# Kernel optimization log

Hardware: AMD Instinct MI355X
Metric: run time of the kernel (lower is better)

## Reference

```python
import jax, jax.numpy as jnp
import numpy as np

N_NODES = 50000
N_EDGES = 800000
N_FEAT = 128
DIM = 64
N_GRAPHS = 512


def setup_inputs() -> dict:
    key = jax.random.key(0)
    k1, k2, k3, k4, k5, k6 = jax.random.split(key, 6)
    x = jax.random.normal(k1, (N_NODES, N_FEAT), dtype=jnp.float32)
    edge_index = jax.random.randint(k2, (2, N_EDGES), 0, N_NODES, dtype=jnp.int64)
    batch = jnp.sort(jax.random.randint(k3, (N_NODES,), 0, N_GRAPHS, dtype=jnp.int64))
    W1 = jax.random.normal(k4, (N_FEAT, DIM), dtype=jnp.float32) * 0.05
    W2 = jax.random.normal(k5, (DIM, DIM), dtype=jnp.float32) * 0.05
    Wfc = jax.random.normal(k6, (DIM, 1), dtype=jnp.float32) * 0.05
    return {"x": x, "edge_index": edge_index, "batch": batch,
            "W1": W1, "W2": W2, "Wfc": Wfc}


def _gcn_conv(h, src, dst, W):
    # GCNConv(normalize=False, bias=False): linear transform then scatter-add
    # over edges: out[dst] += (h @ W)[src]
    h = jnp.einsum('nf,fd->nd', h, W)
    return jax.ops.segment_sum(h[src], dst, num_segments=N_NODES)


def reference(x, edge_index, batch, W1, W2, Wfc):
    src, dst = edge_index[0], edge_index[1]
    h = jax.nn.relu(_gcn_conv(x, src, dst, W1))          # [N, DIM]
    h = _gcn_conv(h, src, dst, W2)                        # [N, DIM]
    # global_mean_pool over graph ids
    counts = jax.ops.segment_sum(jnp.ones((N_NODES,), h.dtype), batch,
                                 num_segments=N_GRAPHS)   # [G]
    pooled = jax.ops.segment_sum(h, batch, num_segments=N_GRAPHS)
    pooled = pooled / jnp.maximum(counts, 1.0)[:, None]   # [G, DIM]
    return jax.nn.sigmoid(pooled @ Wfc)                   # [G, 1]
```

## Files before the change

### kernel.cpp

```cpp
#include <hip/hip_runtime.h>
#include <cmath>

#define N_NODES 50000
#define N_EDGES 800000
#define N_FEAT 128
#define DIM 64
#define N_GRAPHS 512
#define GGRID ((N_NODES + 63) / 64)
#define NBKT GGRID
#define BH_BLK 128
#define EPB (N_EDGES / BH_BLK)
#define NCNT (NBKT * BH_BLK)
#define P2_NBLK ((NCNT + 511) / 512)
#define BKT_CAP 2048

__device__ __forceinline__ unsigned short f2bf(float f) {
  union { float f; unsigned int u; } v; v.f = f;
  return (unsigned short)((v.u + 0x7FFFu + ((v.u >> 16) & 1u)) >> 16);
}
__device__ __forceinline__ float bf2f(unsigned short u) {
  union { unsigned int u; float f; } v; v.u = (unsigned int)u << 16;
  return v.f;
}

__global__ __launch_bounds__(256) void bhist_w2fc(const int* __restrict__ dst,
                                                  int* __restrict__ cnt,
                                                  const float* __restrict__ W2,
                                                  const float* __restrict__ Wfc,
                                                  float* __restrict__ w2fc) {
  if (blockIdx.x == BH_BLK) {
    int k = threadIdx.x;
    if (k < 64) {
      float s = 0.f;
#pragma unroll 8
      for (int j = 0; j < 64; j++) s += W2[k * 64 + j] * Wfc[j];
      w2fc[k] = s;
    }
    return;
  }
  __shared__ int lh[NBKT];
  const int tid = threadIdx.x, k = blockIdx.x;
  for (int i = tid; i < NBKT; i += 256) lh[i] = 0;
  __syncthreads();
  const int base = k * EPB;
  for (int j = tid; j < EPB; j += 256)
    atomicAdd(&lh[dst[base + j] >> 6], 1);
  __syncthreads();
  for (int i = tid; i < NBKT; i += 256) cnt[i * BH_BLK + k] = lh[i];
}

__global__ __launch_bounds__(512) void psum512(const int* __restrict__ cnt,
                                               int* __restrict__ partials) {
  __shared__ int ws[8];
  int gid = blockIdx.x * 512 + threadIdx.x;
  int v = (gid < NCNT) ? cnt[gid] : 0;
#pragma unroll
  for (int off = 32; off; off >>= 1) v += __shfl_down(v, off, 64);
  int lane = threadIdx.x & 63, w = threadIdx.x >> 6;
  if (lane == 0) ws[w] = v;
  __syncthreads();
  if (threadIdx.x == 0) {
    int s = 0;
#pragma unroll
    for (int i = 0; i < 8; i++) s += ws[i];
    partials[blockIdx.x] = s;
  }
}

__global__ __launch_bounds__(256) void scan_partials(int* __restrict__ partials) {
  __shared__ int buf[256];
  int tid = threadIdx.x;
  int v = (tid < P2_NBLK) ? partials[tid] : 0;
  buf[tid] = v;
  __syncthreads();
  for (int off = 1; off < 256; off <<= 1) {
    int t = (tid >= off) ? buf[tid - off] : 0;
    __syncthreads();
    buf[tid] += t;
    __syncthreads();
  }
  if (tid < P2_NBLK) partials[tid] = buf[tid] - v;
}

__global__ __launch_bounds__(512) void sblocks512(int* __restrict__ cnt,
                                                  const int* __restrict__ partials,
                                                  int* __restrict__ bucket_ptr) {
  __shared__ int buf[512];
  int tid = threadIdx.x;
  int gid = blockIdx.x * 512 + tid;
  int v = (gid < NCNT) ? cnt[gid] : 0;
  buf[tid] = v;
  __syncthreads();
  for (int off = 1; off < 512; off <<= 1) {
    int t = (tid >= off) ? buf[tid - off] : 0;
    __syncthreads();
    buf[tid] += t;
    __syncthreads();
  }
  int excl = buf[tid] - v + partials[blockIdx.x];
  if (gid < NCNT) {
    cnt[gid] = excl;
    if ((gid & (BH_BLK - 1)) == 0) bucket_ptr[gid / BH_BLK] = excl;
    if (gid == NCNT - 1) bucket_ptr[NBKT] = excl + v;
  }
}

template<int K>
__device__ __forceinline__ void gemm_body_bf(const float* __restrict__ A,
                                             const float* __restrict__ W,
                                             unsigned short* __restrict__ out,
                                             int M, int row0, int tid,
                                             float* sX, float* sW) {
  const int tx = tid & 15, ty = tid >> 4;
  const int q = tid & 7, r0 = tid >> 3;
  float acc[4][4] = {};

  for (int kb = 0; kb < K; kb += 32) {
    __syncthreads();
    if ((kb & 63) == 0) {
#pragma unroll
      for (int i = 0; i < 16; i++)
        sW[i * 256 + tid] = W[kb * 64 + i * 256 + tid];
    }
#pragma unroll
    for (int rr = 0; rr < 64; rr += 32) {
      int r = r0 + rr;
      int gr = row0 + r;
      float4 v = make_float4(0.f, 0.f, 0.f, 0.f);
      if (gr < M) v = *(const float4*)&A[(size_t)gr * K + kb + q * 4];
      *(float4*)&sX[r * 36 + q * 4] = v;
    }
    __syncthreads();

    const int kw = kb & 63;
#pragma unroll 4
    for (int k = 0; k < 32; k += 4) {
      float4 wv[4];
#pragma unroll
      for (int kk = 0; kk < 4; kk++)
        wv[kk] = *(const float4*)&sW[(kw + k + kk) * 64 + tx * 4];
#pragma unroll
      for (int r = 0; r < 4; r++) {
        float4 xv = *(const float4*)&sX[(ty * 4 + r) * 36 + k];
        const float xs[4] = {xv.x, xv.y, xv.z, xv.w};
#pragma unroll
        for (int kk = 0; kk < 4; kk++) {
          acc[r][0] += xs[kk] * wv[kk].x;
          acc[r][1] += xs[kk] * wv[kk].y;
          acc[r][2] += xs[kk] * wv[kk].z;
          acc[r][3] += xs[kk] * wv[kk].w;
        }
      }
    }
  }

#pragma unroll
  for (int r = 0; r < 4; r++) {
    int gr = row0 + ty * 4 + r;
    if (gr < M) {
      ushort4 u;
      u.x = f2bf(acc[r][0]); u.y = f2bf(acc[r][1]);
      u.z = f2bf(acc[r][2]); u.w = f2bf(acc[r][3]);
      *(ushort4*)&out[(size_t)gr * 64 + tx * 4] = u;
    }
  }
}

__global__ __launch_bounds__(256) void gemm1_bscatter(
    const float* __restrict__ x, const float* __restrict__ W1,
    unsigned short* __restrict__ h1, const int* __restrict__ src,
    const int* __restrict__ dst, const int* __restrict__ cnt,
    unsigned int* __restrict__ ebuf) {
  __shared__ float sX[64 * 36];
  __shared__ float sW[64 * 64];
  const int tid = threadIdx.x;
  if (blockIdx.x < GGRID) {
    gemm_body_bf<N_FEAT>(x, W1, h1, N_NODES, blockIdx.x * 64, tid, sX, sW);
  } else {
    int* loff = (int*)sX;
    const int k = blockIdx.x - GGRID;
    for (int i = tid; i < NBKT; i += 256) loff[i] = cnt[i * BH_BLK + k];
    __syncthreads();
    const int base = k * EPB;
    for (int j = tid; j < EPB; j += 256) {
      int e = base + j;
      int d = dst[e];
      int pos = atomicAdd(&loff[d >> 6], 1);
      ebuf[pos] = ((unsigned int)src[e] << 6) | (unsigned int)(d & 63);
    }
  }
}

__global__ __launch_bounds__(1024, 8) void gather_z_fused(
    const unsigned short* __restrict__ h1,
    const unsigned int* __restrict__ ebuf,
    const int* __restrict__ bucket_ptr,
    const float* __restrict__ w2fc,
    float* __restrict__ z) {
  __shared__ int colL[BKT_CAP];
  __shared__ int lstart[64];
  __shared__ int lcur[64];
  __shared__ float sw[64];
  const int tid = threadIdx.x;
  const int b = blockIdx.x;
  const int p0 = bucket_ptr[b];
  int cnt = bucket_ptr[b + 1] - p0;
  if (cnt > BKT_CAP) cnt = BKT_CAP;

  if (tid < 64) { lstart[tid] = 0; sw[tid] = w2fc[tid]; }
  __syncthreads();
  for (int i = tid; i < cnt; i += 1024)
    atomicAdd(&lstart[ebuf[p0 + i] & 63], 1);
  __syncthreads();
  if (tid < 64) {
    int v = lstart[tid], s = v;
#pragma unroll
    for (int off = 1; off < 64; off <<= 1) {
      int t = __shfl_up(s, off, 64);
      if (tid >= off) s += t;
    }
    lstart[tid] = s - v;
    lcur[tid] = s - v;
  }
  __syncthreads();
  for (int i = tid; i < cnt; i += 1024) {
    unsigned int u = ebuf[p0 + i];
    int pos = atomicAdd(&lcur[u & 63], 1);
    colL[pos] = (int)(u >> 6);
  }
  __syncthreads();

  const int lane = tid & 63, w = tid >> 6;
  const int eo = lane >> 4, qfo = (lane & 15) << 2;
#pragma unroll
  for (int ni = 0; ni < 4; ni++) {
    const int r = ni * 16 + w;
    const int i1 = lcur[r];
    int i = lstart[r];
    float4 acc = make_float4(0.f, 0.f, 0.f, 0.f);
    for (; i + 16 <= i1; i += 16) {
      int s0 = colL[i + eo];
      int s1 = colL[i + 4 + eo];
      int s2 = colL[i + 8 + eo];
      int s3 = colL[i + 12 + eo];
      ushort4 u0 = *(const ushort4*)&h1[(size_t)s0 * 64 + qfo];
      ushort4 u1 = *(const ushort4*)&h1[(size_t)s1 * 64 + qfo];
      ushort4 u2 = *(const ushort4*)&h1[(size_t)s2 * 64 + qfo];
      ushort4 u3 = *(const ushort4*)&h1[(size_t)s3 * 64 + qfo];
      acc.x += (bf2f(u0.x) + bf2f(u1.x)) + (bf2f(u2.x) + bf2f(u3.x));
      acc.y += (bf2f(u0.y) + bf2f(u1.y)) + (bf2f(u2.y) + bf2f(u3.y));
      acc.z += (bf2f(u0.z) + bf2f(u1.z)) + (bf2f(u2.z) + bf2f(u3.z));
      acc.w += (bf2f(u0.w) + bf2f(u1.w)) + (bf2f(u2.w) + bf2f(u3.w));
    }
    for (; i + 4 <= i1; i += 4) {
      int s = colL[i + eo];
      ushort4 u = *(const ushort4*)&h1[(size_t)s * 64 + qfo];
      acc.x += bf2f(u.x); acc.y += bf2f(u.y);
      acc.z += bf2f(u.z); acc.w += bf2f(u.w);
    }
    if (eo < i1 - i) {
      int s = colL[i + eo];
      ushort4 u = *(const ushort4*)&h1[(size_t)s * 64 + qfo];
      acc.x += bf2f(u.x); acc.y += bf2f(u.y);
      acc.z += bf2f(u.z); acc.w += bf2f(u.w);
    }
#pragma unroll
    for (int m = 16; m <= 32; m <<= 1) {
      acc.x += __shfl_xor(acc.x, m, 64);
      acc.y += __shfl_xor(acc.y, m, 64);
      acc.z += __shfl_xor(acc.z, m, 64);
      acc.w += __shfl_xor(acc.w, m, 64);
    }
    float p = fmaxf(acc.x, 0.f) * sw[qfo] + fmaxf(acc.y, 0.f) * sw[qfo + 1] +
              fmaxf(acc.z, 0.f) * sw[qfo + 2] + fmaxf(acc.w, 0.f) * sw[qfo + 3];
#pragma unroll
    for (int m = 1; m <= 8; m <<= 1) p += __shfl_xor(p, m, 64);
    int node = b * 64 + r;
    if (lane == 0 && node < N_NODES) z[node] = p;
  }
}

__global__ __launch_bounds__(256) void graph_pool(const float* __restrict__ z,
                                                  const unsigned int* __restrict__ ebuf,
                                                  const int* __restrict__ bucket_ptr,
                                                  const int* __restrict__ batch,
                                                  float* __restrict__ out) {
  __shared__ float sacc[4];
  int g = blockIdx.x;
  int tid = threadIdx.x, lane = tid & 63, w = tid >> 6;

  int lo = 0, hi = N_NODES;
  while (lo < hi) { int mid = (lo + hi) >> 1; if (batch[mid] < g) lo = mid + 1; else hi = mid; }
  const int start = lo;
  hi = N_NODES;
  while (lo < hi) { int mid = (lo + hi) >> 1; if (batch[mid] < g + 1) lo = mid + 1; else hi = mid; }
  const int end = lo;

  float s = 0.f;
  if (end > start) {
    const int b0 = start >> 6, b1 = ((end - 1) >> 6) + 1;
    for (int b = b0; b < b1; b++) {
      const int q0 = bucket_ptr[b], q1 = bucket_ptr[b + 1];
      const int base = b << 6;
      for (int i = q0 + tid; i < q1; i += 256) {
        unsigned int u = ebuf[i];
        int d = base + (int)(u & 63);
        if (d >= start && d < end) s += z[u >> 6];
      }
    }
  }
#pragma unroll
  for (int off = 32; off; off >>= 1) s += __shfl_down(s, off, 64);
  if (lane == 0) sacc[w] = s;
  __syncthreads();
  if (tid == 0) {
    float v = sacc[0] + sacc[1] + sacc[2] + sacc[3];
    v /= fmaxf((float)(end - start), 1.f);
    out[g] = 1.f / (1.f + expf(-v));
  }
}

extern "C" void kernel_launch(void* const* d_in, const int* in_sizes, int n_in,
                              void* d_out, int out_size, void* d_ws, size_t ws_size,
                              hipStream_t stream) {
  const float* x     = (const float*)d_in[0];
  const int*   ei    = (const int*)d_in[1];
  const int*   batch = (const int*)d_in[2];
  const float* W1    = (const float*)d_in[3];
  const float* W2    = (const float*)d_in[4];
  const float* Wfc   = (const float*)d_in[5];
  float*       out   = (float*)d_out;

  const int* src = ei;
  const int* dst = ei + N_EDGES;

  char* ws = (char*)d_ws;
  unsigned short* h1 = (unsigned short*)(ws);
  float* z    = (float*)(ws + (size_t)N_NODES * DIM * 2);
  float* w2fc = z + N_NODES;
  int*   cnt  = (int*)(w2fc + 64);
  int*   partials = cnt + NCNT;
  unsigned int* ebuf = (unsigned int*)(partials + P2_NBLK);
  int*   bucket_ptr  = (int*)(ebuf + N_EDGES);

  bhist_w2fc<<<BH_BLK + 1, 256, 0, stream>>>(dst, cnt, W2, Wfc, w2fc);
  psum512<<<P2_NBLK, 512, 0, stream>>>(cnt, partials);
  scan_partials<<<1, 256, 0, stream>>>(partials);
  sblocks512<<<P2_NBLK, 512, 0, stream>>>(cnt, partials, bucket_ptr);

  gemm1_bscatter<<<GGRID + BH_BLK, 256, 0, stream>>>(x, W1, h1, src, dst, cnt, ebuf);

  gather_z_fused<<<NBKT, 1024, 0, stream>>>(h1, ebuf, bucket_ptr, w2fc, z);

  graph_pool<<<N_GRAPHS, 256, 0, stream>>>(z, ebuf, bucket_ptr, batch, out);
}
```

Measured before the change: 151.4 us.

## Spread GEMM1 tiles across the sort-preparation kernels and merge the partial scan

Splits the 782 GEMM1 row tiles across the histogram, partial-sum, block-scan and scatter launches, so the otherwise underfilled small kernels also do matrix work alongside their main job. The separate single-block partials scan is removed; each scan block now recomputes the prefix over the partials itself. The count reduction and scan switch to 256-thread blocks that each handle two counters via int2 loads. The tile split is hardcoded (262+160+160+200 = 782) and must match GGRID exactly, and the scan blocks repeat work on the partials.

New measurement: 159.6 us. 1.05x slower.

```diff
diff --git a/kernel.cpp b/kernel.cpp
--- a/kernel.cpp
+++ b/kernel.cpp
@@ -14,6 +14,11 @@
 #define P2_NBLK ((NCNT + 511) / 512)
 #define BKT_CAP 2048
 
+#define T_BHIST 262
+#define T_PSUM  160
+#define T_SBLK  160
+#define T_BSCAT 200
+
 __device__ __forceinline__ unsigned short f2bf(float f) {
   union { float f; unsigned int u; } v; v.f = f;
   return (unsigned short)((v.u + 0x7FFFu + ((v.u >> 16) & 1u)) >> 16);
@@ -21,88 +26,6 @@
 __device__ __forceinline__ float bf2f(unsigned short u) {
   union { unsigned int u; float f; } v; v.u = (unsigned int)u << 16;
   return v.f;
-}
-
-__global__ __launch_bounds__(256) void bhist_w2fc(const int* __restrict__ dst,
-                                                  int* __restrict__ cnt,
-                                                  const float* __restrict__ W2,
-                                                  const float* __restrict__ Wfc,
-                                                  float* __restrict__ w2fc) {
-  if (blockIdx.x == BH_BLK) {
-    int k = threadIdx.x;
-    if (k < 64) {
-      float s = 0.f;
-#pragma unroll 8
-      for (int j = 0; j < 64; j++) s += W2[k * 64 + j] * Wfc[j];
-      w2fc[k] = s;
-    }
-    return;
-  }
-  __shared__ int lh[NBKT];
-  const int tid = threadIdx.x, k = blockIdx.x;
-  for (int i = tid; i < NBKT; i += 256) lh[i] = 0;
-  __syncthreads();
-  const int base = k * EPB;
-  for (int j = tid; j < EPB; j += 256)
-    atomicAdd(&lh[dst[base + j] >> 6], 1);
-  __syncthreads();
-  for (int i = tid; i < NBKT; i += 256) cnt[i * BH_BLK + k] = lh[i];
-}
-
-__global__ __launch_bounds__(512) void psum512(const int* __restrict__ cnt,
-                                               int* __restrict__ partials) {
-  __shared__ int ws[8];
-  int gid = blockIdx.x * 512 + threadIdx.x;
-  int v = (gid < NCNT) ? cnt[gid] : 0;
-#pragma unroll
-  for (int off = 32; off; off >>= 1) v += __shfl_down(v, off, 64);
-  int lane = threadIdx.x & 63, w = threadIdx.x >> 6;
-  if (lane == 0) ws[w] = v;
-  __syncthreads();
-  if (threadIdx.x == 0) {
-    int s = 0;
-#pragma unroll
-    for (int i = 0; i < 8; i++) s += ws[i];
-    partials[blockIdx.x] = s;
-  }
-}
-
-__global__ __launch_bounds__(256) void scan_partials(int* __restrict__ partials) {
-  __shared__ int buf[256];
-  int tid = threadIdx.x;
-  int v = (tid < P2_NBLK) ? partials[tid] : 0;
-  buf[tid] = v;
-  __syncthreads();
-  for (int off = 1; off < 256; off <<= 1) {
-    int t = (tid >= off) ? buf[tid - off] : 0;
-    __syncthreads();
-    buf[tid] += t;
-    __syncthreads();
-  }
-  if (tid < P2_NBLK) partials[tid] = buf[tid] - v;
-}
-
-__global__ __launch_bounds__(512) void sblocks512(int* __restrict__ cnt,
-                                                  const int* __restrict__ partials,
-                                                  int* __restrict__ bucket_ptr) {
-  __shared__ int buf[512];
-  int tid = threadIdx.x;
-  int gid = blockIdx.x * 512 + tid;
-  int v = (gid < NCNT) ? cnt[gid] : 0;
-  buf[tid] = v;
-  __syncthreads();
-  for (int off = 1; off < 512; off <<= 1) {
-    int t = (tid >= off) ? buf[tid - off] : 0;
-    __syncthreads();
-    buf[tid] += t;
-    __syncthreads();
-  }
-  int excl = buf[tid] - v + partials[blockIdx.x];
-  if (gid < NCNT) {
-    cnt[gid] = excl;
-    if ((gid & (BH_BLK - 1)) == 0) bucket_ptr[gid / BH_BLK] = excl;
-    if (gid == NCNT - 1) bucket_ptr[NBKT] = excl + v;
-  }
 }
 
 template<int K>
@@ -166,28 +89,136 @@
   }
 }
 
-__global__ __launch_bounds__(256) void gemm1_bscatter(
-    const float* __restrict__ x, const float* __restrict__ W1,
-    unsigned short* __restrict__ h1, const int* __restrict__ src,
-    const int* __restrict__ dst, const int* __restrict__ cnt,
-    unsigned int* __restrict__ ebuf) {
+__global__ __launch_bounds__(256) void f_bhist(const int* __restrict__ dst,
+                                               int* __restrict__ cnt,
+                                               const float* __restrict__ W2,
+                                               const float* __restrict__ Wfc,
+                                               float* __restrict__ w2fc,
+                                               const float* __restrict__ x,
+                                               const float* __restrict__ W1,
+                                               unsigned short* __restrict__ h1) {
   __shared__ float sX[64 * 36];
   __shared__ float sW[64 * 64];
   const int tid = threadIdx.x;
-  if (blockIdx.x < GGRID) {
-    gemm_body_bf<N_FEAT>(x, W1, h1, N_NODES, blockIdx.x * 64, tid, sX, sW);
-  } else {
-    int* loff = (int*)sX;
-    const int k = blockIdx.x - GGRID;
-    for (int i = tid; i < NBKT; i += 256) loff[i] = cnt[i * BH_BLK + k];
+  if (blockIdx.x >= BH_BLK + 1) {
+    int tile = blockIdx.x - (BH_BLK + 1);
+    gemm_body_bf<N_FEAT>(x, W1, h1, N_NODES, tile * 64, tid, sX, sW);
+    return;
+  }
+  if (blockIdx.x == BH_BLK) {
+    if (tid < 64) {
+      float s = 0.f;
+#pragma unroll 8
+      for (int j = 0; j < 64; j++) s += W2[tid * 64 + j] * Wfc[j];
+      w2fc[tid] = s;
+    }
+    return;
+  }
+  int* lh = (int*)sX;
+  const int k = blockIdx.x;
+  for (int i = tid; i < NBKT; i += 256) lh[i] = 0;
+  __syncthreads();
+  const int base = k * EPB;
+  for (int j = tid; j < EPB; j += 256)
+    atomicAdd(&lh[dst[base + j] >> 6], 1);
+  __syncthreads();
+  for (int i = tid; i < NBKT; i += 256) cnt[i * BH_BLK + k] = lh[i];
+}
+
+__global__ __launch_bounds__(256) void f_psum(const int* __restrict__ cnt,
+                                              int* __restrict__ partials,
+                                              const float* __restrict__ x,
+                                              const float* __restrict__ W1,
+                                              unsigned short* __restrict__ h1) {
+  __shared__ float sX[64 * 36];
+  __shared__ float sW[64 * 64];
+  const int tid = threadIdx.x;
+  if (blockIdx.x >= P2_NBLK) {
+    int tile = T_BHIST + (blockIdx.x - P2_NBLK);
+    gemm_body_bf<N_FEAT>(x, W1, h1, N_NODES, tile * 64, tid, sX, sW);
+    return;
+  }
+  int* ws = (int*)sX;
+  const int2* cnt2 = (const int2*)cnt;
+  int idx = blockIdx.x * 256 + tid;
+  int v = 0;
+  if (idx * 2 < NCNT) { int2 c = cnt2[idx]; v = c.x + c.y; }
+#pragma unroll
+  for (int off = 32; off; off >>= 1) v += __shfl_down(v, off, 64);
+  int lane = tid & 63, w = tid >> 6;
+  if (lane == 0) ws[w] = v;
+  __syncthreads();
+  if (tid == 0) partials[blockIdx.x] = ws[0] + ws[1] + ws[2] + ws[3];
+}
+
+__global__ __launch_bounds__(256) void f_sblocks(int* __restrict__ cnt,
+                                                 const int* __restrict__ partials,
+                                                 int* __restrict__ bucket_ptr,
+                                                 const float* __restrict__ x,
+                                                 const float* __restrict__ W1,
+                                                 unsigned short* __restrict__ h1) {
+  __shared__ float sX[64 * 36];
+  __shared__ float sW[64 * 64];
+  const int tid = threadIdx.x;
+  if (blockIdx.x >= P2_NBLK) {
+    int tile = T_BHIST + T_PSUM + (blockIdx.x - P2_NBLK);
+    gemm_body_bf<N_FEAT>(x, W1, h1, N_NODES, tile * 64, tid, sX, sW);
+    return;
+  }
+  int* buf  = (int*)sX;
+  int* pbuf = buf + 256;
+  int2* cnt2 = (int2*)cnt;
+  const int idx = blockIdx.x * 256 + tid;
+  int2 c = make_int2(0, 0);
+  if (idx * 2 < NCNT) c = cnt2[idx];
+  int s = c.x + c.y;
+  buf[tid] = s;
+  pbuf[tid] = (tid < P2_NBLK) ? partials[tid] : 0;
+  __syncthreads();
+  for (int off = 1; off < 256; off <<= 1) {
+    int t1 = (tid >= off) ? buf[tid - off] : 0;
+    int t2 = (tid >= off) ? pbuf[tid - off] : 0;
     __syncthreads();
-    const int base = k * EPB;
-    for (int j = tid; j < EPB; j += 256) {
-      int e = base + j;
-      int d = dst[e];
-      int pos = atomicAdd(&loff[d >> 6], 1);
-      ebuf[pos] = ((unsigned int)src[e] << 6) | (unsigned int)(d & 63);
-    }
+    buf[tid] += t1;
+    pbuf[tid] += t2;
+    __syncthreads();
+  }
+  const int thr_excl = buf[tid] - s;
+  const int base = (blockIdx.x > 0) ? pbuf[blockIdx.x - 1] : 0;
+  if (idx * 2 < NCNT) {
+    int e0 = base + thr_excl;
+    cnt2[idx] = make_int2(e0, e0 + c.x);
+    int p = idx * 2;
+    if ((p & (BH_BLK - 1)) == 0) bucket_ptr[p >> 7] = e0;
+    if (p + 1 == NCNT - 1) bucket_ptr[NBKT] = e0 + c.x + c.y;
+  }
+}
+
+__global__ __launch_bounds__(256) void f_bscatter(const int* __restrict__ src,
+                                                  const int* __restrict__ dst,
+                                                  const int* __restrict__ cnt,
+                                                  unsigned int* __restrict__ ebuf,
+                                                  const float* __restrict__ x,
+                                                  const float* __restrict__ W1,
+                                                  unsigned short* __restrict__ h1) {
+  __shared__ float sX[64 * 36];
+  __shared__ float sW[64 * 64];
+  const int tid = threadIdx.x;
+  if (blockIdx.x >= BH_BLK) {
+    int tile = T_BHIST + T_PSUM + T_SBLK + (blockIdx.x - BH_BLK);
+    gemm_body_bf<N_FEAT>(x, W1, h1, N_NODES, tile * 64, tid, sX, sW);
+    return;
+  }
+  int* loff = (int*)sX;
+  const int k = blockIdx.x;
+  for (int i = tid; i < NBKT; i += 256) loff[i] = cnt[i * BH_BLK + k];
+  __syncthreads();
+  const int base = k * EPB;
+  for (int j = tid; j < EPB; j += 256) {
+    int e = base + j;
+    int d = dst[e];
+    int pos = atomicAdd(&loff[d >> 6], 1);
+    ebuf[pos] = ((unsigned int)src[e] << 6) | (unsigned int)(d & 63);
   }
 }
 
@@ -343,12 +374,13 @@
   unsigned int* ebuf = (unsigned int*)(partials + P2_NBLK);
   int*   bucket_ptr  = (int*)(ebuf + N_EDGES);
 
-  bhist_w2fc<<<BH_BLK + 1, 256, 0, stream>>>(dst, cnt, W2, Wfc, w2fc);
-  psum512<<<P2_NBLK, 512, 0, stream>>>(cnt, partials);
-  scan_partials<<<1, 256, 0, stream>>>(partials);
-  sblocks512<<<P2_NBLK, 512, 0, stream>>>(cnt, partials, bucket_ptr);
-
-  gemm1_bscatter<<<GGRID + BH_BLK, 256, 0, stream>>>(x, W1, h1, src, dst, cnt, ebuf);
+  f_bhist<<<BH_BLK + 1 + T_BHIST, 256, 0, stream>>>(dst, cnt, W2, Wfc, w2fc,
+                                                    x, W1, h1);
+  f_psum<<<P2_NBLK + T_PSUM, 256, 0, stream>>>(cnt, partials, x, W1, h1);
+  f_sblocks<<<P2_NBLK + T_SBLK, 256, 0, stream>>>(cnt, partials, bucket_ptr,
+                                                  x, W1, h1);
+  f_bscatter<<<BH_BLK + T_BSCAT, 256, 0, stream>>>(src, dst, cnt, ebuf,
+                                                   x, W1, h1);
 
   gather_z_fused<<<NBKT, 1024, 0, stream>>>(h1, ebuf, bucket_ptr, w2fc, z);
 
```
